# Performance work log

Hardware: AMD Instinct MI355X
Metric: run time of the kernel (lower is better)

Reference implementation:

```python
import jax, jax.numpy as jnp
import numpy as np


def _gelu(v):
    return jax.nn.gelu(v, approximate=False)


def _conv1x1(x, W, b):
    # x: [B, Ci, H, W], W: [Co, Ci]
    return jnp.einsum('bixy,oi->boxy', x, W) + b[None, :, None, None]


def _spectral(x, w1r, w2r, m1, m2):
    # x: [B, Ci, H, W]; w*r: [Ci, Co, m1, m2, 2] (real/imag)
    w1 = w1r[..., 0] + 1j * w1r[..., 1]
    w2 = w2r[..., 0] + 1j * w2r[..., 1]
    B, C, H, W = x.shape
    xf = jnp.fft.rfft2(x)  # [B, Ci, H, W//2+1] complex64
    o1 = jnp.einsum('bixy,ioxy->boxy', xf[:, :, :m1, :m2], w1)
    o2 = jnp.einsum('bixy,ioxy->boxy', xf[:, :, H - m1:, :m2], w2)
    Co = w1.shape[1]
    of = jnp.zeros((B, Co, H, W // 2 + 1), dtype=xf.dtype)
    of = of.at[:, :, :m1, :m2].set(o1)
    of = of.at[:, :, H - m1:, :m2].set(o2)
    return jnp.fft.irfft2(of, s=(H, W))


def _pool(x):
    B, C, H, W = x.shape
    return x.reshape(B, C, H // 2, 2, W // 2, 2).mean(axis=(3, 5))


def _up(x):
    # matches torch F.interpolate(scale_factor=2, mode='bilinear', align_corners=False)
    B, C, H, W = x.shape
    return jax.image.resize(x, (B, C, 2 * H, 2 * W), method='bilinear')


def _forward(x, fcin_w, fcin_b, sc1_w1, sc1_w2, c1_w, c1_b, sc2_w1, sc2_w2, c2_w, c2_b,
             scb_w1, scb_w2, cb_w, cb_b, su2_w1, su2_w2, u2_w, u2_b,
             su1_w1, su1_w2, u1_w, u1_b, fc1_w, fc1_b, fc2_w, fc2_b):
    v = jnp.einsum('bhwi,oi->bhwo', x, fcin_w) + fcin_b   # lift 6 -> width
    v = v.transpose(0, 3, 1, 2)                            # [B, C, H, W]
    x1 = _gelu(_spectral(v, sc1_w1, sc1_w2, 12, 12) + _conv1x1(v, c1_w, c1_b))
    x1d = _pool(x1)
    x2 = _gelu(_spectral(x1d, sc2_w1, sc2_w2, 8, 8) + _conv1x1(x1d, c2_w, c2_b))
    x2d = _pool(x2)
    xb = _gelu(_spectral(x2d, scb_w1, scb_w2, 4, 4) + _conv1x1(x2d, cb_w, cb_b))
    x2c = jnp.concatenate([_up(xb), x2], axis=1)           # [B, 3.5w, H/2, W/2]
    x2o = _gelu(_spectral(x2c, su2_w1, su2_w2, 8, 8) + _conv1x1(x2c, u2_w, u2_b))
    x1c = jnp.concatenate([_up(x2o), x1], axis=1)          # [B, 2.5w, H, W]
    x1o = _gelu(_spectral(x1c, su1_w1, su1_w2, 12, 12) + _conv1x1(x1c, u1_w, u1_b))
    h = x1o.transpose(0, 2, 3, 1)
    h = _gelu(jnp.einsum('bhwi,oi->bhwo', h, fc1_w) + fc1_b)
    return jnp.einsum('bhwi,oi->bhwo', h, fc2_w) + fc2_b   # [B, H, W, 3]


def setup_inputs() -> dict:
    key = jax.random.key(0)
    ks = jax.random.split(key, 20)

    def cw(k, ci, co, m):  # complex spectral weight stored as [...,2] real
        return (1.0 / (ci * co)) * jax.random.normal(k, (ci, co, m, m, 2), dtype=jnp.float32)

    def lin(k, o, i):
        k1, k2 = jax.random.split(k)
        lim = 1.0 / np.sqrt(i)
        return (jax.random.uniform(k1, (o, i), jnp.float32, -lim, lim),
                jax.random.uniform(k2, (o,), jnp.float32, -lim, lim))

    d = {}
    d['x'] = jax.random.normal(ks[0], (4, 256, 256, 6), dtype=jnp.float32)
    d['fcin_w'], d['fcin_b'] = lin(ks[1], 64, 6)
    d['sc1_w1'] = cw(ks[2], 64, 64, 12); d['sc1_w2'] = cw(ks[3], 64, 64, 12)
    d['c1_w'], d['c1_b'] = lin(ks[4], 64, 64)
    d['sc2_w1'] = cw(ks[5], 64, 96, 8); d['sc2_w2'] = cw(ks[6], 64, 96, 8)
    d['c2_w'], d['c2_b'] = lin(ks[7], 96, 64)
    d['scb_w1'] = cw(ks[8], 96, 128, 4); d['scb_w2'] = cw(ks[9], 96, 128, 4)
    d['cb_w'], d['cb_b'] = lin(ks[10], 128, 96)
    d['su2_w1'] = cw(ks[11], 224, 96, 8); d['su2_w2'] = cw(ks[12], 224, 96, 8)
    d['u2_w'], d['u2_b'] = lin(ks[13], 96, 224)
    d['su1_w1'] = cw(ks[14], 160, 64, 12); d['su1_w2'] = cw(ks[15], 160, 64, 12)
    d['u1_w'], d['u1_b'] = lin(ks[16], 64, 160)
    d['fc1_w'], d['fc1_b'] = lin(ks[17], 256, 64)
    d['fc2_w'], d['fc2_b'] = lin(ks[18], 3, 256)
    return d


def reference(x, fcin_w, fcin_b, sc1_w1, sc1_w2, c1_w, c1_b, sc2_w1, sc2_w2, c2_w, c2_b,
              scb_w1, scb_w2, cb_w, cb_b, su2_w1, su2_w2, u2_w, u2_b,
              su1_w1, su1_w2, u1_w, u1_b, fc1_w, fc1_b, fc2_w, fc2_b):
    return _forward(x, fcin_w, fcin_b, sc1_w1, sc1_w2, c1_w, c1_b, sc2_w1, sc2_w2, c2_w, c2_b,
                    scb_w1, scb_w2, cb_w, cb_b, su2_w1, su2_w2, u2_w, u2_b,
                    su1_w1, su1_w2, u1_w, u1_b, fc1_w, fc1_b, fc2_w, fc2_b)
```

## Files before the change

kernel.cpp:

```cpp
#include <hip/hip_runtime.h>
#include <math.h>
#include <cstdio>


__device__ __forceinline__ float gelu_f(float v) {
    return 0.5f * v * (1.0f + erff(v * 0.70710678118654752f));
}

__global__ __launch_bounds__(256) void init_tw_kernel(float2* tw) {
    int t = threadIdx.x;
    tw[t] = make_float2(cospif(t * (1.0f / 128.0f)), sinpif(t * (1.0f / 128.0f)));
}

__global__ __launch_bounds__(256) void transpose_mat_kernel(const float* __restrict__ src,
                                                            float* __restrict__ dst,
                                                            int Co, int Ci) {
    int idx = blockIdx.x * blockDim.x + threadIdx.x;
    if (idx >= Ci * Co) return;
    int o = idx % Co; int i = idx / Co;
    dst[idx] = src[(size_t)o * Ci + i];
}

template <int M2, int SRC, int W_T>
__global__ __launch_bounds__(256, 4) void dftx_kernel(
    const float* __restrict__ U, int C, int Coff, int Ctot,
    int H, int Hs, int Ws,
    const float* __restrict__ liftW, const float* __restrict__ liftB,
    int stepW, const float2* __restrict__ tw, float2* __restrict__ Fx) {
    constexpr int W = W_T;
    constexpr int WS2 = W_T / 2;
    __shared__ float2 twxk[(SRC == 2) ? (WS2 * M2) : (W * M2)];
    int tid = threadIdx.x;
    if constexpr (SRC == 2) {
        for (int t = tid; t < WS2 * M2; t += 256) {
            int j = t / M2, k = t - (t / M2) * M2;
            float wr = 0.f, wi = 0.f;
            auto addE = [&](int xx, float w) {
                float2 e = tw[(xx * k * stepW) & 255];
                wr += w * e.x; wi += w * e.y;
            };
            if (j == 0)            { addE(0, 1.0f); addE(1, 0.75f); addE(2, 0.25f); }
            else if (j == WS2 - 1) { addE(2 * j - 1, 0.25f); addE(2 * j, 0.75f); addE(2 * j + 1, 1.0f); }
            else                   { addE(2 * j - 1, 0.25f); addE(2 * j, 0.75f);
                                     addE(2 * j + 1, 0.75f); addE(2 * j + 2, 0.25f); }
            twxk[t] = make_float2(wr, wi);
        }
    } else {
        for (int t = tid; t < W * M2; t += 256) {
            int x = t / M2, k = t - (t / M2) * M2;
            twxk[t] = tw[(x * k * stepW) & 255];
        }
    }
    __syncthreads();
    int by = blockIdx.x * 4 + (tid >> 6);
    int c = blockIdx.y * 64 + (tid & 63);
    if (c >= C) return;

    const float* rowD = nullptr;
    const float* Sa = nullptr; const float* Sb = nullptr;
    float wy = 0.f, bc = 0.f;
    float w6[6] = {0, 0, 0, 0, 0, 0};
    if constexpr (SRC == 0) {
        rowD = U + (size_t)by * W * C + c;
    } else if constexpr (SRC == 1) {
        bc = liftB[c];
#pragma unroll
        for (int j = 0; j < 6; j++) w6[j] = liftW[c * 6 + j];
    } else {
        int b = by / H, y = by % H;
        float fy = 0.5f * y - 0.25f;
        int y0 = (int)floorf(fy); wy = fy - y0;
        int ya = y0 < 0 ? 0 : y0;
        int yb = (y0 + 1 > Hs - 1) ? Hs - 1 : y0 + 1;
        Sa = U + ((size_t)(b * Hs + ya) * Ws) * C + c;
        Sb = U + ((size_t)(b * Hs + yb) * Ws) * C + c;
    }

    float ar[M2], ai[M2];
#pragma unroll
    for (int k = 0; k < M2; k++) { ar[k] = 0.f; ai[k] = 0.f; }
    if constexpr (SRC == 2) {
        for (int js = 0; js < WS2; js++) {
            float sa = Sa[(size_t)js * C], sb = Sb[(size_t)js * C];
            float u = sa * (1.f - wy) + sb * wy;
            const float4* gp = (const float4*)&twxk[js * M2];
#pragma unroll
            for (int k2 = 0; k2 < M2 / 2; k2++) {
                float4 g4 = gp[k2];
                ar[2 * k2] += u * g4.x;     ai[2 * k2] -= u * g4.y;
                ar[2 * k2 + 1] += u * g4.z; ai[2 * k2 + 1] -= u * g4.w;
            }
        }
    } else {
        for (int x = 0; x < W; x++) {
            float u;
            if constexpr (SRC == 0) {
                u = rowD[(size_t)x * C];
            } else {
                const float* xp = U + ((size_t)by * W + x) * 6;
                u = bc;
#pragma unroll
                for (int j = 0; j < 6; j++) u += w6[j] * xp[j];
            }
            const float4* wp = (const float4*)&twxk[x * M2];
#pragma unroll
            for (int k2 = 0; k2 < M2 / 2; k2++) {
                float4 t4 = wp[k2];
                ar[2 * k2] += u * t4.x;     ai[2 * k2] -= u * t4.y;
                ar[2 * k2 + 1] += u * t4.z; ai[2 * k2 + 1] -= u * t4.w;
            }
        }
    }
    float2* o = Fx + ((size_t)by * M2) * Ctot + Coff + c;
#pragma unroll
    for (int k = 0; k < M2; k++) o[(size_t)k * Ctot] = make_float2(ar[k], ai[k]);
}

template <int M1>
__global__ __launch_bounds__(256, 2) void dfty2_kernel(
    const float2* __restrict__ Fx, int H, int m2, int Ct,
    int stepH, const float2* __restrict__ tw, float2* __restrict__ XF) {
    constexpr int NKY = 2 * M1;
    __shared__ float twc[256], tws[256];
    __shared__ float2 red[3][NKY][64];
    int tid = threadIdx.x;
    for (int t = tid; t < 256; t += 256) {
        float2 v = tw[t]; twc[t] = v.x; tws[t] = v.y;
    }
    __syncthreads();
    int kx = blockIdx.x % m2; int ct = blockIdx.x / m2;
    int b = blockIdx.y;
    int lane = tid & 63, grp = tid >> 6;
    int c = ct * 64 + lane;
    float ar[NKY], ai[NKY];
#pragma unroll
    for (int k = 0; k < NKY; k++) { ar[k] = 0.f; ai[k] = 0.f; }
    if (c < Ct) {
        int ylen = H >> 2;
        int y0 = grp * ylen;
        const float2* base = Fx + ((size_t)(b * H + y0) * m2 + kx) * Ct + c;
        size_t stride = (size_t)m2 * Ct;
        for (int yy = 0; yy < ylen; yy++) {
            float2 f = base[(size_t)yy * stride];
            int a = ((y0 + yy) * stepH) & 255;
            int t = 0;
#pragma unroll
            for (int j = 0; j < M1; j++) {
                float cc = twc[t], ss = tws[t];
                ar[j] += f.x * cc + f.y * ss;
                ai[j] += f.y * cc - f.x * ss;
                t = (t + a) & 255;
            }
            t = (M1 * 256 - M1 * a) & 255;
#pragma unroll
            for (int j = 0; j < M1; j++) {
                float cc = twc[t], ss = tws[t];
                ar[M1 + j] += f.x * cc + f.y * ss;
                ai[M1 + j] += f.y * cc - f.x * ss;
                t = (t + a) & 255;
            }
        }
    }
    if (grp > 0) {
#pragma unroll
        for (int k = 0; k < NKY; k++) red[grp - 1][k][lane] = make_float2(ar[k], ai[k]);
    }
    __syncthreads();
    if (grp == 0 && c < Ct) {
#pragma unroll
        for (int k = 0; k < NKY; k++) {
            float2 r0 = red[0][k][lane], r1 = red[1][k][lane], r2 = red[2][k][lane];
            XF[((size_t)(b * NKY + k) * m2 + kx) * Ct + c] =
                make_float2(ar[k] + r0.x + r1.x + r2.x, ai[k] + r0.y + r1.y + r2.y);
        }
    }
}

__global__ __launch_bounds__(128, 2) void modemix2_kernel(
    const float2* __restrict__ XF,
    const float* __restrict__ w1f, const float* __restrict__ w2f,
    int Ci, int Co, int m1, int m2, float2* __restrict__ OF) {
    __shared__ float2 xsm[4][224];
    int mode = blockIdx.x;
    int nmode = 2 * m1 * m2;
    for (int t = threadIdx.x; t < 4 * Ci; t += blockDim.x) {
        int b = t / Ci, i = t - b * Ci;
        xsm[b][i] = XF[((size_t)b * nmode + mode) * Ci + i];
    }
    __syncthreads();
    int o = threadIdx.x;
    if (o >= Co) return;
    int kx = mode % m2; int kyi = mode / m2;
    const float2* w = (const float2*)((kyi < m1) ? w1f : w2f);
    int ky = (kyi < m1) ? kyi : (kyi - m1);
    float ar0 = 0, ai0 = 0, ar1 = 0, ai1 = 0, ar2 = 0, ai2 = 0, ar3 = 0, ai3 = 0;
    for (int i = 0; i < Ci; i++) {
        float2 wv = w[(((size_t)i * Co + o) * m1 + ky) * m2 + kx];
        float2 a = xsm[0][i], b2 = xsm[1][i], c2 = xsm[2][i], d2 = xsm[3][i];
        ar0 += a.x * wv.x - a.y * wv.y;  ai0 += a.x * wv.y + a.y * wv.x;
        ar1 += b2.x * wv.x - b2.y * wv.y; ai1 += b2.x * wv.y + b2.y * wv.x;
        ar2 += c2.x * wv.x - c2.y * wv.y; ai2 += c2.x * wv.y + c2.y * wv.x;
        ar3 += d2.x * wv.x - d2.y * wv.y; ai3 += d2.x * wv.y + d2.y * wv.x;
    }
    OF[((size_t)0 * nmode + mode) * Co + o] = make_float2(ar0, ai0);
    OF[((size_t)1 * nmode + mode) * Co + o] = make_float2(ar1, ai1);
    OF[((size_t)2 * nmode + mode) * Co + o] = make_float2(ar2, ai2);
    OF[((size_t)3 * nmode + mode) * Co + o] = make_float2(ar3, ai3);
}

__global__ __launch_bounds__(256, 4) void idfty_kernel(
    const float2* __restrict__ OF, int H, int m1, int m2, int Co,
    int stepH, const float2* __restrict__ tw, float2* __restrict__ Gy, int N) {
    __shared__ float twc[256], tws[256];
    for (int t = threadIdx.x; t < 256; t += blockDim.x) {
        float2 v = tw[t]; twc[t] = v.x; tws[t] = v.y;
    }
    __syncthreads();
    int idx = blockIdx.x * blockDim.x + threadIdx.x;
    if (idx >= N) return;
    int o = idx % Co; int r = idx / Co;
    int kx = r % m2;  r /= m2;
    int y = r % H;    int b = r / H;
    float accr = 0.f, acci = 0.f;
    for (int kyi = 0; kyi < 2 * m1; kyi++) {
        int ky = (kyi < m1) ? kyi : (H - 2 * m1 + kyi);
        int t = (ky * y * stepH) & 255;
        float2 f = OF[((size_t)(b * 2 * m1 + kyi) * m2 + kx) * Co + o];
        float cc = twc[t], ss = tws[t];
        accr += f.x * cc - f.y * ss;
        acci += f.x * ss + f.y * cc;
    }
    Gy[idx] = make_float2(accr, acci);
}

template <int SRCA, bool HASB, int CO, int CI, int M2, int MINW>
__global__ __launch_bounds__((CO / 4) * 8, MINW) void synth_kernel(
    const float2* __restrict__ Gy,
    const float* __restrict__ A, int CA, int HsA, int WsA,
    const float* __restrict__ UB, int CB,
    const float* __restrict__ liftW, const float* __restrict__ liftB,
    const float* __restrict__ WcT, const float* __restrict__ bias,
    int H, int W, int stepW, float invHW,
    const float2* __restrict__ tw, float* __restrict__ out) {
    constexpr int OQ = CO / 4;
    constexpr int BLK = OQ * 8;
    constexpr int P = 32;
    constexpr int CIH = CI / 2;
    constexpr int CIP = CI + 1;
    __shared__ float xs[P][CIP];
    __shared__ float2 twL[M2][P];
    int tid = threadIdx.x;
    int pix0 = blockIdx.x * P;
    int x0 = pix0 % W;  int by = pix0 / W;
    for (int t = tid; t < M2 * P; t += BLK) {
        int k = t / P, p = t - (t / P) * P;
        float2 v = tw[((x0 + p) * k * stepW) & 255];
        float s = ((k == 0) ? 1.f : 2.f) * invHW;
        twL[k][p] = make_float2(s * v.x, s * v.y);
    }
    for (int t = tid; t < P * CI; t += BLK) {
        int p = t / CI, i = t - p * CI;
        int pix = pix0 + p;
        float val;
        if (HASB && i >= CA) {
            val = UB[(size_t)pix * CB + (i - CA)];
        } else if constexpr (SRCA == 0) {
            val = A[(size_t)pix * CA + i];
        } else if constexpr (SRCA == 1) {
            const float* xp = A + (size_t)pix * 6;
            float a = liftB[i];
#pragma unroll
            for (int j = 0; j < 6; j++) a += xp[j] * liftW[i * 6 + j];
            val = a;
        } else {
            int xx = pix % W; int r = pix / W; int y = r % H; int b = r / H;
            float fy = 0.5f * y - 0.25f, fx = 0.5f * xx - 0.25f;
            int y0 = (int)floorf(fy); float wy = fy - y0;
            int x0i = (int)floorf(fx); float wx = fx - x0i;
            int ya = y0 < 0 ? 0 : y0;
            int yb = (y0 + 1 > HsA - 1) ? HsA - 1 : y0 + 1;
            int xa = x0i < 0 ? 0 : x0i;
            int xb2 = (x0i + 1 > WsA - 1) ? WsA - 1 : x0i + 1;
            const float* base = A + ((size_t)b * HsA * WsA) * CA + i;
            float v00 = base[((size_t)ya * WsA + xa) * CA];
            float v01 = base[((size_t)ya * WsA + xb2) * CA];
            float v10 = base[((size_t)yb * WsA + xa) * CA];
            float v11 = base[((size_t)yb * WsA + xb2) * CA];
            val = (1.f - wy) * ((1.f - wx) * v00 + wx * v01) +
                  wy * ((1.f - wx) * v10 + wx * v11);
        }
        xs[p][i] = val;
    }
    __syncthreads();
    int oq = tid % OQ, pg = tid / OQ;
    float acc[4][4];
#pragma unroll
    for (int q = 0; q < 4; q++)
#pragma unroll
        for (int j = 0; j < 4; j++) acc[q][j] = 0.f;
    const float2* grow = Gy + ((size_t)by * M2) * CO + oq * 4;
#pragma unroll
    for (int k = 0; k < M2; k++) {
        float4 ga = *(const float4*)&grow[(size_t)k * CO];
        float4 gb = *(const float4*)&grow[(size_t)k * CO + 2];
#pragma unroll
        for (int q = 0; q < 4; q++) {
            float2 tq = twL[k][pg * 4 + q];
            acc[q][0] += ga.x * tq.x - ga.y * tq.y;
            acc[q][1] += ga.z * tq.x - ga.w * tq.y;
            acc[q][2] += gb.x * tq.x - gb.y * tq.y;
            acc[q][3] += gb.z * tq.x - gb.w * tq.y;
        }
    }
    const float* w0p = WcT + oq * 4;
    const float* w1p = WcT + (size_t)CIH * CO + oq * 4;
#pragma unroll 4
    for (int il = 0; il < CIH; il++) {
        float4 wa = *(const float4*)&w0p[(size_t)il * CO];
        float4 wb = *(const float4*)&w1p[(size_t)il * CO];
#pragma unroll
        for (int q = 0; q < 4; q++) {
            float a0 = xs[pg * 4 + q][il];
            float a1 = xs[pg * 4 + q][CIH + il];
            acc[q][0] += a0 * wa.x + a1 * wb.x;
            acc[q][1] += a0 * wa.y + a1 * wb.y;
            acc[q][2] += a0 * wa.z + a1 * wb.z;
            acc[q][3] += a0 * wa.w + a1 * wb.w;
        }
    }
    float4 bb = *(const float4*)&bias[oq * 4];
#pragma unroll
    for (int q = 0; q < 4; q++) {
        int pix = pix0 + pg * 4 + q;
        float4 r;
        r.x = gelu_f(acc[q][0] + bb.x);
        r.y = gelu_f(acc[q][1] + bb.y);
        r.z = gelu_f(acc[q][2] + bb.z);
        r.w = gelu_f(acc[q][3] + bb.w);
        *(float4*)&out[(size_t)pix * CO + oq * 4] = r;
    }
}

__global__ __launch_bounds__(256, 2) void head_kernel(
    const float* __restrict__ xin, const float* __restrict__ fc1t,
    const float* __restrict__ fc1b, const float* __restrict__ fc2w,
    const float* __restrict__ fc2b, float* __restrict__ out) {
    __shared__ float xs[16][65];
    __shared__ float red[64][49];
    int tid = threadIdx.x;
    int pix0 = blockIdx.x * 16;
    const float* src = xin + (size_t)pix0 * 64;
    for (int t = tid; t < 16 * 64; t += 256) xs[t >> 6][t & 63] = src[t];
    __syncthreads();
    int jq = tid & 63, pg = tid >> 6;
    float acc[4][4];
#pragma unroll
    for (int q = 0; q < 4; q++)
#pragma unroll
        for (int j = 0; j < 4; j++) acc[q][j] = 0.f;
    const float* wrow = fc1t + jq * 4;
#pragma unroll 4
    for (int i = 0; i < 32; i++) {
        float4 wa = *(const float4*)&wrow[(size_t)i * 256];
        float4 wb = *(const float4*)&wrow[(size_t)(i + 32) * 256];
#pragma unroll
        for (int q = 0; q < 4; q++) {
            float a0 = xs[pg * 4 + q][i];
            float a1 = xs[pg * 4 + q][i + 32];
            acc[q][0] += a0 * wa.x + a1 * wb.x;
            acc[q][1] += a0 * wa.y + a1 * wb.y;
            acc[q][2] += a0 * wa.z + a1 * wb.z;
            acc[q][3] += a0 * wa.w + a1 * wb.w;
        }
    }
    float4 b1 = *(const float4*)&fc1b[jq * 4];
    float4 w20 = *(const float4*)&fc2w[0 * 256 + jq * 4];
    float4 w21 = *(const float4*)&fc2w[1 * 256 + jq * 4];
    float4 w22 = *(const float4*)&fc2w[2 * 256 + jq * 4];
#pragma unroll
    for (int q = 0; q < 4; q++) {
        float h0 = gelu_f(acc[q][0] + b1.x);
        float h1 = gelu_f(acc[q][1] + b1.y);
        float h2 = gelu_f(acc[q][2] + b1.z);
        float h3 = gelu_f(acc[q][3] + b1.w);
        int col = (pg * 4 + q) * 3;
        red[jq][col + 0] = h0 * w20.x + h1 * w20.y + h2 * w20.z + h3 * w20.w;
        red[jq][col + 1] = h0 * w21.x + h1 * w21.y + h2 * w21.z + h3 * w21.w;
        red[jq][col + 2] = h0 * w22.x + h1 * w22.y + h2 * w22.z + h3 * w22.w;
    }
    __syncthreads();
    if (tid < 48) {
        float s = 0.f;
        for (int j = 0; j < 64; j++) s += red[j][tid];
        int px = tid / 3, o3 = tid - 3 * px;
        out[(size_t)(pix0 + px) * 3 + o3] = s + fc2b[o3];
    }
}

__global__ __launch_bounds__(256, 4) void pool_kernel(
    const float* __restrict__ in, float* __restrict__ out,
    int H2, int W2, int C, int N) {
    int idx = blockIdx.x * blockDim.x + threadIdx.x;
    if (idx >= N) return;
    int c = idx % C; int r = idx / C;
    int xo = r % W2; r /= W2;
    int yo = r % H2; int b = r / H2;
    int W = W2 * 2;
    const float* p = in + (((size_t)(b * (H2 * 2) + 2 * yo) * W) + 2 * xo) * C + c;
    float v = p[0] + p[C] + p[(size_t)W * C] + p[(size_t)W * C + C];
    out[idx] = 0.25f * v;
}


static inline unsigned nb_(size_t n, int b) { return (unsigned)((n + b - 1) / b); }

extern "C" void kernel_launch(void* const* d_in, const int* in_sizes, int n_in,
                              void* d_out, int out_size, void* d_ws, size_t ws_size,
                              hipStream_t stream) {
    (void)in_sizes; (void)n_in; (void)out_size;
    const float* x      = (const float*)d_in[0];
    const float* fcin_w = (const float*)d_in[1];
    const float* fcin_b = (const float*)d_in[2];
    const float* sc1_w1 = (const float*)d_in[3];
    const float* sc1_w2 = (const float*)d_in[4];
    const float* c1_w   = (const float*)d_in[5];
    const float* c1_b   = (const float*)d_in[6];
    const float* sc2_w1 = (const float*)d_in[7];
    const float* sc2_w2 = (const float*)d_in[8];
    const float* c2_w   = (const float*)d_in[9];
    const float* c2_b   = (const float*)d_in[10];
    const float* scb_w1 = (const float*)d_in[11];
    const float* scb_w2 = (const float*)d_in[12];
    const float* cb_w   = (const float*)d_in[13];
    const float* cb_b   = (const float*)d_in[14];
    const float* su2_w1 = (const float*)d_in[15];
    const float* su2_w2 = (const float*)d_in[16];
    const float* u2_w   = (const float*)d_in[17];
    const float* u2_b   = (const float*)d_in[18];
    const float* su1_w1 = (const float*)d_in[19];
    const float* su1_w2 = (const float*)d_in[20];
    const float* u1_w   = (const float*)d_in[21];
    const float* u1_b   = (const float*)d_in[22];
    const float* fc1_w  = (const float*)d_in[23];
    const float* fc1_b  = (const float*)d_in[24];
    const float* fc2_w  = (const float*)d_in[25];
    const float* fc2_b  = (const float*)d_in[26];
    float* out = (float*)d_out;

    float* wsf = (float*)d_ws;
    size_t off = 0;
    auto alloc = [&](size_t nfloats) -> float* {
        float* p = wsf + off;
        off += (nfloats + 63) & ~(size_t)63;
        return p;
    };

    float2* tw = (float2*)alloc(512);
    float* c1t  = alloc(64 * 64);
    float* c2t  = alloc(64 * 96);
    float* cbt  = alloc(96 * 128);
    float* u2t  = alloc(224 * 96);
    float* u1t  = alloc(160 * 64);
    float* fc1t = alloc(64 * 256);

    float* x1  = alloc((size_t)4 * 256 * 256 * 64);
    float* x1d = alloc((size_t)4 * 128 * 128 * 64);
    float* x2  = alloc((size_t)4 * 128 * 128 * 96);
    float* xb  = alloc((size_t)4 * 64 * 64 * 128);
    float* x2o = alloc((size_t)4 * 128 * 128 * 96);

    float2* Fx = (float2*)alloc((size_t)2 * 4 * 256 * 12 * 160);
    float2* XF = (float2*)alloc((size_t)2 * 4 * 24 * 12 * 160);
    float2* OF = (float2*)alloc((size_t)2 * 4 * 24 * 12 * 128);
    float2* Gy = (float2*)alloc((size_t)2 * 4 * 256 * 12 * 96);

    size_t need = off * sizeof(float);
    if (ws_size < need) {
        fprintf(stderr, "[FNO2d] workspace too small: need %zu bytes, have %zu\n",
                need, ws_size);
        return;
    }
    float* x2d = x1d;

    init_tw_kernel<<<1, 256, 0, stream>>>(tw);
    transpose_mat_kernel<<<nb_(64 * 64, 256), 256, 0, stream>>>(c1_w, c1t, 64, 64);
    transpose_mat_kernel<<<nb_(64 * 96, 256), 256, 0, stream>>>(c2_w, c2t, 96, 64);
    transpose_mat_kernel<<<nb_(96 * 128, 256), 256, 0, stream>>>(cb_w, cbt, 128, 96);
    transpose_mat_kernel<<<nb_(224 * 96, 256), 256, 0, stream>>>(u2_w, u2t, 96, 224);
    transpose_mat_kernel<<<nb_(160 * 64, 256), 256, 0, stream>>>(u1_w, u1t, 64, 160);
    transpose_mat_kernel<<<nb_(64 * 256, 256), 256, 0, stream>>>(fc1_w, fc1t, 256, 64);

    int N;

    dftx_kernel<12, 1, 256><<<dim3(256, 1), 256, 0, stream>>>(
        x, 64, 0, 64, 256, 0, 0, fcin_w, fcin_b, 1, tw, Fx);
    dfty2_kernel<12><<<dim3(12, 4), 256, 0, stream>>>(Fx, 256, 12, 64, 1, tw, XF);
    modemix2_kernel<<<288, 128, 0, stream>>>(XF, sc1_w1, sc1_w2, 64, 64, 12, 12, OF);
    N = 4 * 256 * 12 * 64;
    idfty_kernel<<<nb_(N, 256), 256, 0, stream>>>(OF, 256, 12, 12, 64, 1, tw, Gy, N);
    synth_kernel<1, false, 64, 64, 12, 3><<<4 * 256 * 256 / 32, 128, 0, stream>>>(
        Gy, x, 64, 0, 0, nullptr, 0, fcin_w, fcin_b, c1t, c1_b,
        256, 256, 1, 1.0f / 65536.0f, tw, x1);
    N = 4 * 128 * 128 * 64;
    pool_kernel<<<nb_(N, 256), 256, 0, stream>>>(x1, x1d, 128, 128, 64, N);

    dftx_kernel<8, 0, 128><<<dim3(128, 1), 256, 0, stream>>>(
        x1d, 64, 0, 64, 128, 0, 0, nullptr, nullptr, 2, tw, Fx);
    dfty2_kernel<8><<<dim3(8, 4), 256, 0, stream>>>(Fx, 128, 8, 64, 2, tw, XF);
    modemix2_kernel<<<128, 128, 0, stream>>>(XF, sc2_w1, sc2_w2, 64, 96, 8, 8, OF);
    N = 4 * 128 * 8 * 96;
    idfty_kernel<<<nb_(N, 256), 256, 0, stream>>>(OF, 128, 8, 8, 96, 2, tw, Gy, N);
    synth_kernel<0, false, 96, 64, 8, 3><<<4 * 128 * 128 / 32, 192, 0, stream>>>(
        Gy, x1d, 64, 0, 0, nullptr, 0, nullptr, nullptr, c2t, c2_b,
        128, 128, 2, 1.0f / 16384.0f, tw, x2);
    N = 4 * 64 * 64 * 96;
    pool_kernel<<<nb_(N, 256), 256, 0, stream>>>(x2, x2d, 64, 64, 96, N);

    dftx_kernel<4, 0, 64><<<dim3(64, 2), 256, 0, stream>>>(
        x2d, 96, 0, 96, 64, 0, 0, nullptr, nullptr, 4, tw, Fx);
    dfty2_kernel<4><<<dim3(4 * 2, 4), 256, 0, stream>>>(Fx, 64, 4, 96, 4, tw, XF);
    modemix2_kernel<<<32, 128, 0, stream>>>(XF, scb_w1, scb_w2, 96, 128, 4, 4, OF);
    N = 4 * 64 * 4 * 128;
    idfty_kernel<<<nb_(N, 256), 256, 0, stream>>>(OF, 64, 4, 4, 128, 4, tw, Gy, N);
    synth_kernel<0, false, 128, 96, 4, 2><<<4 * 64 * 64 / 32, 256, 0, stream>>>(
        Gy, x2d, 96, 0, 0, nullptr, 0, nullptr, nullptr, cbt, cb_b,
        64, 64, 4, 1.0f / 4096.0f, tw, xb);

    dftx_kernel<8, 2, 128><<<dim3(128, 2), 256, 0, stream>>>(
        xb, 128, 0, 224, 128, 64, 64, nullptr, nullptr, 2, tw, Fx);
    dftx_kernel<8, 0, 128><<<dim3(128, 2), 256, 0, stream>>>(
        x2, 96, 128, 224, 128, 0, 0, nullptr, nullptr, 2, tw, Fx);
    dfty2_kernel<8><<<dim3(8 * 4, 4), 256, 0, stream>>>(Fx, 128, 8, 224, 2, tw, XF);
    modemix2_kernel<<<128, 128, 0, stream>>>(XF, su2_w1, su2_w2, 224, 96, 8, 8, OF);
    N = 4 * 128 * 8 * 96;
    idfty_kernel<<<nb_(N, 256), 256, 0, stream>>>(OF, 128, 8, 8, 96, 2, tw, Gy, N);
    synth_kernel<2, true, 96, 224, 8, 2><<<4 * 128 * 128 / 32, 192, 0, stream>>>(
        Gy, xb, 128, 64, 64, x2, 96, nullptr, nullptr, u2t, u2_b,
        128, 128, 2, 1.0f / 16384.0f, tw, x2o);

    dftx_kernel<12, 2, 256><<<dim3(256, 2), 256, 0, stream>>>(
        x2o, 96, 0, 160, 256, 128, 128, nullptr, nullptr, 1, tw, Fx);
    dftx_kernel<12, 0, 256><<<dim3(256, 1), 256, 0, stream>>>(
        x1, 64, 96, 160, 256, 0, 0, nullptr, nullptr, 1, tw, Fx);
    dfty2_kernel<12><<<dim3(12 * 3, 4), 256, 0, stream>>>(Fx, 256, 12, 160, 1, tw, XF);
    modemix2_kernel<<<288, 128, 0, stream>>>(XF, su1_w1, su1_w2, 160, 64, 12, 12, OF);
    N = 4 * 256 * 12 * 64;
    idfty_kernel<<<nb_(N, 256), 256, 0, stream>>>(OF, 256, 12, 12, 64, 1, tw, Gy, N);
    synth_kernel<2, true, 64, 160, 12, 3><<<4 * 256 * 256 / 32, 128, 0, stream>>>(
        Gy, x2o, 96, 128, 128, x1, 64, nullptr, nullptr, u1t, u1_b,
        256, 256, 1, 1.0f / 65536.0f, tw, x1);

    head_kernel<<<4 * 256 * 256 / 16, 256, 0, stream>>>(
        x1, fc1t, fc1_b, fc2_w, fc2_b, out);
}
```

Measured before the change: 1.790 ms.

## Split dfty over row slices with a separate reduction kernel; simplify 1x1 loops

The column DFT kernel is split across YS row slices, so each block sums only a fraction of the rows and writes partial sums to a new buffer. A small reduction kernel then adds the slices. This raises block counts from tiny grids (e.g. 48 blocks) towards full GPU occupancy, at the cost of an extra launch and partial-buffer traffic. Separately, the 1x1-conv inner loops in synth and head are rewritten from a two-half split into a single sequential loop over input channels.

Measured after the change: 1.678 ms. -6.3%, faster.

```diff
diff --git a/kernel.cpp b/kernel.cpp
--- a/kernel.cpp
+++ b/kernel.cpp
@@ -116,10 +116,10 @@
     for (int k = 0; k < M2; k++) o[(size_t)k * Ctot] = make_float2(ar[k], ai[k]);
 }
 
-template <int M1>
-__global__ __launch_bounds__(256, 2) void dfty2_kernel(
+template <int M1, int YS>
+__global__ __launch_bounds__(256, 2) void dfty3_kernel(
     const float2* __restrict__ Fx, int H, int m2, int Ct,
-    int stepH, const float2* __restrict__ tw, float2* __restrict__ XF) {
+    int stepH, const float2* __restrict__ tw, float2* __restrict__ XFp) {
     constexpr int NKY = 2 * M1;
     __shared__ float twc[256], tws[256];
     __shared__ float2 red[3][NKY][64];
@@ -129,18 +129,19 @@
     }
     __syncthreads();
     int kx = blockIdx.x % m2; int ct = blockIdx.x / m2;
-    int b = blockIdx.y;
+    int ys = blockIdx.y % YS; int b = blockIdx.y / YS;
     int lane = tid & 63, grp = tid >> 6;
     int c = ct * 64 + lane;
     float ar[NKY], ai[NKY];
 #pragma unroll
     for (int k = 0; k < NKY; k++) { ar[k] = 0.f; ai[k] = 0.f; }
     if (c < Ct) {
-        int ylen = H >> 2;
-        int y0 = grp * ylen;
+        int rows = H / YS;
+        int sub = rows / 4;
+        int y0 = ys * rows + grp * sub;
         const float2* base = Fx + ((size_t)(b * H + y0) * m2 + kx) * Ct + c;
         size_t stride = (size_t)m2 * Ct;
-        for (int yy = 0; yy < ylen; yy++) {
+        for (int yy = 0; yy < sub; yy++) {
             float2 f = base[(size_t)yy * stride];
             int a = ((y0 + yy) * stepH) & 255;
             int t = 0;
@@ -170,10 +171,29 @@
 #pragma unroll
         for (int k = 0; k < NKY; k++) {
             float2 r0 = red[0][k][lane], r1 = red[1][k][lane], r2 = red[2][k][lane];
-            XF[((size_t)(b * NKY + k) * m2 + kx) * Ct + c] =
+            XFp[(((size_t)(b * YS + ys) * NKY + k) * m2 + kx) * Ct + c] =
                 make_float2(ar[k] + r0.x + r1.x + r2.x, ai[k] + r0.y + r1.y + r2.y);
         }
     }
+}
+
+__global__ __launch_bounds__(256, 4) void dfty_reduce_kernel(
+    const float2* __restrict__ XFp, float2* __restrict__ XF,
+    int nky, int m2, int Ct, int YS, int N) {
+    int idx = blockIdx.x * blockDim.x + threadIdx.x;
+    if (idx >= N) return;
+    int c = idx % Ct; int r = idx / Ct;
+    int kx = r % m2;  r /= m2;
+    int k = r % nky;  int b = r / nky;
+    size_t inner = (((size_t)k) * m2 + kx) * Ct + c;
+    size_t bstride = (size_t)nky * m2 * Ct;
+    const float2* p = XFp + (size_t)b * YS * bstride + inner;
+    float sr = 0.f, si = 0.f;
+    for (int ys = 0; ys < YS; ys++) {
+        float2 v = p[(size_t)ys * bstride];
+        sr += v.x; si += v.y;
+    }
+    XF[idx] = make_float2(sr, si);
 }
 
 __global__ __launch_bounds__(128, 2) void modemix2_kernel(
@@ -245,7 +265,6 @@
     constexpr int OQ = CO / 4;
     constexpr int BLK = OQ * 8;
     constexpr int P = 32;
-    constexpr int CIH = CI / 2;
     constexpr int CIP = CI + 1;
     __shared__ float xs[P][CIP];
     __shared__ float2 twL[M2][P];
@@ -312,20 +331,15 @@
             acc[q][3] += gb.z * tq.x - gb.w * tq.y;
         }
     }
-    const float* w0p = WcT + oq * 4;
-    const float* w1p = WcT + (size_t)CIH * CO + oq * 4;
-#pragma unroll 4
-    for (int il = 0; il < CIH; il++) {
-        float4 wa = *(const float4*)&w0p[(size_t)il * CO];
-        float4 wb = *(const float4*)&w1p[(size_t)il * CO];
+    const float* wrow = WcT + oq * 4;
+#pragma unroll 8
+    for (int i = 0; i < CI; i++) {
+        float4 w = *(const float4*)&wrow[(size_t)i * CO];
 #pragma unroll
         for (int q = 0; q < 4; q++) {
-            float a0 = xs[pg * 4 + q][il];
-            float a1 = xs[pg * 4 + q][CIH + il];
-            acc[q][0] += a0 * wa.x + a1 * wb.x;
-            acc[q][1] += a0 * wa.y + a1 * wb.y;
-            acc[q][2] += a0 * wa.z + a1 * wb.z;
-            acc[q][3] += a0 * wa.w + a1 * wb.w;
+            float a = xs[pg * 4 + q][i];
+            acc[q][0] += a * w.x; acc[q][1] += a * w.y;
+            acc[q][2] += a * w.z; acc[q][3] += a * w.w;
         }
     }
     float4 bb = *(const float4*)&bias[oq * 4];
@@ -359,18 +373,13 @@
 #pragma unroll
         for (int j = 0; j < 4; j++) acc[q][j] = 0.f;
     const float* wrow = fc1t + jq * 4;
-#pragma unroll 4
-    for (int i = 0; i < 32; i++) {
-        float4 wa = *(const float4*)&wrow[(size_t)i * 256];
-        float4 wb = *(const float4*)&wrow[(size_t)(i + 32) * 256];
+    for (int i = 0; i < 64; i++) {
+        float4 w = *(const float4*)&wrow[(size_t)i * 256];
 #pragma unroll
         for (int q = 0; q < 4; q++) {
-            float a0 = xs[pg * 4 + q][i];
-            float a1 = xs[pg * 4 + q][i + 32];
-            acc[q][0] += a0 * wa.x + a1 * wb.x;
-            acc[q][1] += a0 * wa.y + a1 * wb.y;
-            acc[q][2] += a0 * wa.z + a1 * wb.z;
-            acc[q][3] += a0 * wa.w + a1 * wb.w;
+            float a = xs[pg * 4 + q][i];
+            acc[q][0] += a * w.x; acc[q][1] += a * w.y;
+            acc[q][2] += a * w.z; acc[q][3] += a * w.w;
         }
     }
     float4 b1 = *(const float4*)&fc1b[jq * 4];
@@ -469,10 +478,11 @@
     float* xb  = alloc((size_t)4 * 64 * 64 * 128);
     float* x2o = alloc((size_t)4 * 128 * 128 * 96);
 
-    float2* Fx = (float2*)alloc((size_t)2 * 4 * 256 * 12 * 160);
-    float2* XF = (float2*)alloc((size_t)2 * 4 * 24 * 12 * 160);
-    float2* OF = (float2*)alloc((size_t)2 * 4 * 24 * 12 * 128);
-    float2* Gy = (float2*)alloc((size_t)2 * 4 * 256 * 12 * 96);
+    float2* Fx  = (float2*)alloc((size_t)2 * 4 * 256 * 12 * 160);
+    float2* XF  = (float2*)alloc((size_t)2 * 4 * 24 * 12 * 160);
+    float2* XFp = (float2*)alloc((size_t)2 * 4 * 8 * 24 * 12 * 160);
+    float2* OF  = (float2*)alloc((size_t)2 * 4 * 24 * 12 * 128);
+    float2* Gy  = (float2*)alloc((size_t)2 * 4 * 256 * 12 * 96);
 
     size_t need = off * sizeof(float);
     if (ws_size < need) {
@@ -494,7 +504,9 @@
 
     dftx_kernel<12, 1, 256><<<dim3(256, 1), 256, 0, stream>>>(
         x, 64, 0, 64, 256, 0, 0, fcin_w, fcin_b, 1, tw, Fx);
-    dfty2_kernel<12><<<dim3(12, 4), 256, 0, stream>>>(Fx, 256, 12, 64, 1, tw, XF);
+    dfty3_kernel<12, 8><<<dim3(12, 32), 256, 0, stream>>>(Fx, 256, 12, 64, 1, tw, XFp);
+    N = 4 * 24 * 12 * 64;
+    dfty_reduce_kernel<<<nb_(N, 256), 256, 0, stream>>>(XFp, XF, 24, 12, 64, 8, N);
     modemix2_kernel<<<288, 128, 0, stream>>>(XF, sc1_w1, sc1_w2, 64, 64, 12, 12, OF);
     N = 4 * 256 * 12 * 64;
     idfty_kernel<<<nb_(N, 256), 256, 0, stream>>>(OF, 256, 12, 12, 64, 1, tw, Gy, N);
@@ -506,7 +518,9 @@
 
     dftx_kernel<8, 0, 128><<<dim3(128, 1), 256, 0, stream>>>(
         x1d, 64, 0, 64, 128, 0, 0, nullptr, nullptr, 2, tw, Fx);
-    dfty2_kernel<8><<<dim3(8, 4), 256, 0, stream>>>(Fx, 128, 8, 64, 2, tw, XF);
+    dfty3_kernel<8, 8><<<dim3(8, 32), 256, 0, stream>>>(Fx, 128, 8, 64, 2, tw, XFp);
+    N = 4 * 16 * 8 * 64;
+    dfty_reduce_kernel<<<nb_(N, 256), 256, 0, stream>>>(XFp, XF, 16, 8, 64, 8, N);
     modemix2_kernel<<<128, 128, 0, stream>>>(XF, sc2_w1, sc2_w2, 64, 96, 8, 8, OF);
     N = 4 * 128 * 8 * 96;
     idfty_kernel<<<nb_(N, 256), 256, 0, stream>>>(OF, 128, 8, 8, 96, 2, tw, Gy, N);
@@ -518,7 +532,9 @@
 
     dftx_kernel<4, 0, 64><<<dim3(64, 2), 256, 0, stream>>>(
         x2d, 96, 0, 96, 64, 0, 0, nullptr, nullptr, 4, tw, Fx);
-    dfty2_kernel<4><<<dim3(4 * 2, 4), 256, 0, stream>>>(Fx, 64, 4, 96, 4, tw, XF);
+    dfty3_kernel<4, 4><<<dim3(8, 16), 256, 0, stream>>>(Fx, 64, 4, 96, 4, tw, XFp);
+    N = 4 * 8 * 4 * 96;
+    dfty_reduce_kernel<<<nb_(N, 256), 256, 0, stream>>>(XFp, XF, 8, 4, 96, 4, N);
     modemix2_kernel<<<32, 128, 0, stream>>>(XF, scb_w1, scb_w2, 96, 128, 4, 4, OF);
     N = 4 * 64 * 4 * 128;
     idfty_kernel<<<nb_(N, 256), 256, 0, stream>>>(OF, 64, 4, 4, 128, 4, tw, Gy, N);
@@ -530,7 +546,9 @@
         xb, 128, 0, 224, 128, 64, 64, nullptr, nullptr, 2, tw, Fx);
     dftx_kernel<8, 0, 128><<<dim3(128, 2), 256, 0, stream>>>(
         x2, 96, 128, 224, 128, 0, 0, nullptr, nullptr, 2, tw, Fx);
-    dfty2_kernel<8><<<dim3(8 * 4, 4), 256, 0, stream>>>(Fx, 128, 8, 224, 2, tw, XF);
+    dfty3_kernel<8, 8><<<dim3(32, 32), 256, 0, stream>>>(Fx, 128, 8, 224, 2, tw, XFp);
+    N = 4 * 16 * 8 * 224;
+    dfty_reduce_kernel<<<nb_(N, 256), 256, 0, stream>>>(XFp, XF, 16, 8, 224, 8, N);
     modemix2_kernel<<<128, 128, 0, stream>>>(XF, su2_w1, su2_w2, 224, 96, 8, 8, OF);
     N = 4 * 128 * 8 * 96;
     idfty_kernel<<<nb_(N, 256), 256, 0, stream>>>(OF, 128, 8, 8, 96, 2, tw, Gy, N);
@@ -542,7 +560,9 @@
         x2o, 96, 0, 160, 256, 128, 128, nullptr, nullptr, 1, tw, Fx);
     dftx_kernel<12, 0, 256><<<dim3(256, 1), 256, 0, stream>>>(
         x1, 64, 96, 160, 256, 0, 0, nullptr, nullptr, 1, tw, Fx);
-    dfty2_kernel<12><<<dim3(12 * 3, 4), 256, 0, stream>>>(Fx, 256, 12, 160, 1, tw, XF);
+    dfty3_kernel<12, 8><<<dim3(36, 32), 256, 0, stream>>>(Fx, 256, 12, 160, 1, tw, XFp);
+    N = 4 * 24 * 12 * 160;
+    dfty_reduce_kernel<<<nb_(N, 256), 256, 0, stream>>>(XFp, XF, 24, 12, 160, 8, N);
     modemix2_kernel<<<288, 128, 0, stream>>>(XF, su1_w1, su1_w2, 160, 64, 12, 12, OF);
     N = 4 * 256 * 12 * 64;
     idfty_kernel<<<nb_(N, 256), 256, 0, stream>>>(OF, 256, 12, 12, 64, 1, tw, Gy, N);
```
